# Kernel optimization log

Hardware: AMD Instinct MI355X
Metric: run time of the kernel (lower is better)

Reference implementation:

```python
import jax, jax.numpy as jnp
import numpy as np

N = 4096
IN_F = 512
OUT_F = 64
N_HEADS = 8
ALPHA = 0.2
NEG_INF = -9e15


def setup_inputs() -> dict:
    key = jax.random.key(0)
    k1, k2, k3, k4 = jax.random.split(key, 4)
    h = jax.random.normal(k1, (N, IN_F), dtype=jnp.float32)
    adj = jax.random.randint(k2, (N, N), 0, 2, dtype=jnp.int32)
    W = jax.random.normal(k3, (IN_F, OUT_F * N_HEADS), dtype=jnp.float32) * (1.414 / np.sqrt(IN_F))
    a = jax.random.normal(k4, (2 * OUT_F, 1), dtype=jnp.float32) * 0.1
    return {"h": h, "adj": adj, "W": W, "a": a}


def reference(h, adj, W, a):
    # Wh: [N, H, F]
    Wh = (h @ W).reshape(N, N_HEADS, OUT_F)
    # The all-pairs concat + matmul with a ([2F,1], shared across heads)
    # decomposes exactly: e[i,j,h] = leakyrelu(Wh[i,h]@a[:F] + Wh[j,h]@a[F:])
    a_src = a[:OUT_F, 0]
    a_dst = a[OUT_F:, 0]
    src = jnp.einsum('nhf,f->nh', Wh, a_src)  # [N, H]
    dst = jnp.einsum('nhf,f->nh', Wh, a_dst)  # [N, H]
    e = src[:, None, :] + dst[None, :, :]      # [N, N, H]
    e = jnp.where(e > 0, e, ALPHA * e)         # leaky relu
    e = jnp.where(adj[:, :, None] > 0, e, NEG_INF)
    attention = jax.nn.softmax(e, axis=1)      # softmax over neighbors j
    h_prime = jnp.einsum('ijh,jhf->ihf', attention, Wh)  # [N, H, F]
    out = h_prime.reshape(N, N_HEADS * OUT_F)
    return jax.nn.elu(out)
```

## Files before the change

kernel.cpp:

```cpp
#include <hip/hip_runtime.h>
#include <hip/hip_bf16.h>


typedef unsigned short ushort_t;
typedef __attribute__((ext_vector_type(8))) short bf16x8;
typedef __attribute__((ext_vector_type(4))) float f32x4;

#define LOG2E 1.4426950408889634f

__device__ __forceinline__ ushort_t f2bf(float x) {
    unsigned u = __builtin_bit_cast(unsigned, x);
    u += 0x7FFFu + ((u >> 16) & 1u);
    return (ushort_t)(u >> 16);
}

__global__ __launch_bounds__(256) void pack_adj(const int* __restrict__ adj,
                                                unsigned char* __restrict__ pk) {
    int wv = threadIdx.x >> 6, lane = threadIdx.x & 63;
    int row = blockIdx.x * 4 + wv;
    const int* ap = adj + (unsigned)row * 4096 + lane;
    unsigned char* pp = pk + (unsigned)row * 512;
    int jo = lane & 7;
#pragma unroll 2
    for (int k4 = 0; k4 < 16; k4++) {
        int v0 = ap[(k4 * 4 + 0) * 64];
        int v1 = ap[(k4 * 4 + 1) * 64];
        int v2 = ap[(k4 * 4 + 2) * 64];
        int v3 = ap[(k4 * 4 + 3) * 64];
        unsigned long long m0 = __ballot(v0 > 0);
        unsigned long long m1 = __ballot(v1 > 0);
        unsigned long long m2 = __ballot(v2 > 0);
        unsigned long long m3 = __ballot(v3 > 0);
        if (lane < 8) {
            int sh = jo * 8;
            unsigned b = ((unsigned)(m0 >> sh) & 0xFFu)
                       | (((unsigned)(m1 >> sh) & 0xFFu) << 8)
                       | (((unsigned)(m2 >> sh) & 0xFFu) << 16)
                       | (((unsigned)(m3 >> sh) & 0xFFu) << 24);
            *(unsigned*)(pp + jo * 64 + k4 * 4) = b;
        }
    }
}

__global__ __launch_bounds__(256) void transpose_w(const float* __restrict__ W,
                                                   ushort_t* __restrict__ WT) {
    __shared__ ushort_t t[32][33];
    int bx = blockIdx.x & 15, by = blockIdx.x >> 4;
    int tx = threadIdx.x & 31, ty = threadIdx.x >> 5;
#pragma unroll
    for (int i = 0; i < 32; i += 8)
        t[ty + i][tx] = f2bf(W[(by * 32 + ty + i) * 512 + bx * 32 + tx]);
    __syncthreads();
#pragma unroll
    for (int i = 0; i < 32; i += 8)
        WT[(bx * 32 + ty + i) * 512 + by * 32 + tx] = t[tx][ty + i];
}

__global__ __launch_bounds__(256, 4) void gemm_whT(const ushort_t* __restrict__ WT,
                                                   const float* __restrict__ h,
                                                   const float* __restrict__ a,
                                                   ushort_t* __restrict__ WhT,
                                                   float* __restrict__ expA,
                                                   float* __restrict__ expC,
                                                   float* __restrict__ expB,
                                                   float* __restrict__ expD) {
    __shared__ __align__(16) ushort_t Al[2][64][72];
    __shared__ __align__(16) ushort_t Bl[2][64][72];
    __shared__ float asrc[64], adst[64];
    __shared__ float sred[2][4][64];
    int tid = threadIdx.x;
    int wave = tid >> 6, lane = tid & 63, quad = lane >> 4, nn = lane & 15;
    int mb = blockIdx.x & 7, nb = blockIdx.x >> 3;
    if (tid < 64) {
        asrc[tid] = a[tid] * LOG2E;
        adst[tid] = a[64 + tid] * LOG2E;
    }
    int r = tid >> 2, s0 = tid & 3;
    const ushort_t* Ag = WT + (unsigned)((mb * 64 + r) * 512 + s0 * 8);
    const float* Bg = h + (unsigned)((nb * 64 + r) * 512 + s0 * 8);
    bf16x8 pA0 = *(const bf16x8*)(Ag);
    bf16x8 pA1 = *(const bf16x8*)(Ag + 32);
    float4 pb0 = *(const float4*)(Bg);
    float4 pb1 = *(const float4*)(Bg + 4);
    float4 pb2 = *(const float4*)(Bg + 32);
    float4 pb3 = *(const float4*)(Bg + 36);
    f32x4 acc[4] = {};
#pragma unroll 2
    for (int t = 0; t < 8; t++) {
        int cb = t & 1;
        *(bf16x8*)&Al[cb][r][s0 * 8] = pA0;
        *(bf16x8*)&Al[cb][r][s0 * 8 + 32] = pA1;
        bf16x8 bv;
        bv[0] = (short)f2bf(pb0.x); bv[1] = (short)f2bf(pb0.y);
        bv[2] = (short)f2bf(pb0.z); bv[3] = (short)f2bf(pb0.w);
        bv[4] = (short)f2bf(pb1.x); bv[5] = (short)f2bf(pb1.y);
        bv[6] = (short)f2bf(pb1.z); bv[7] = (short)f2bf(pb1.w);
        *(bf16x8*)&Bl[cb][r][s0 * 8] = bv;
        bv[0] = (short)f2bf(pb2.x); bv[1] = (short)f2bf(pb2.y);
        bv[2] = (short)f2bf(pb2.z); bv[3] = (short)f2bf(pb2.w);
        bv[4] = (short)f2bf(pb3.x); bv[5] = (short)f2bf(pb3.y);
        bv[6] = (short)f2bf(pb3.z); bv[7] = (short)f2bf(pb3.w);
        *(bf16x8*)&Bl[cb][r][s0 * 8 + 32] = bv;
        if (t < 7) {
            int ko = (t + 1) * 64;
            pA0 = *(const bf16x8*)(Ag + ko);
            pA1 = *(const bf16x8*)(Ag + ko + 32);
            pb0 = *(const float4*)(Bg + ko);
            pb1 = *(const float4*)(Bg + ko + 4);
            pb2 = *(const float4*)(Bg + ko + 32);
            pb3 = *(const float4*)(Bg + ko + 36);
        }
        if (t > 0) {
            int pb = cb ^ 1;
            bf16x8 af0 = *(const bf16x8*)&Al[pb][wave * 16 + nn][quad * 8];
            bf16x8 af1 = *(const bf16x8*)&Al[pb][wave * 16 + nn][32 + quad * 8];
#pragma unroll
            for (int nt = 0; nt < 4; nt++) {
                bf16x8 b0 = *(const bf16x8*)&Bl[pb][nt * 16 + nn][quad * 8];
                bf16x8 b1 = *(const bf16x8*)&Bl[pb][nt * 16 + nn][32 + quad * 8];
                acc[nt] = __builtin_amdgcn_mfma_f32_16x16x32_bf16(af0, b0, acc[nt], 0, 0, 0);
                acc[nt] = __builtin_amdgcn_mfma_f32_16x16x32_bf16(af1, b1, acc[nt], 0, 0, 0);
            }
        }
        __syncthreads();
    }
    {
        bf16x8 af0 = *(const bf16x8*)&Al[1][wave * 16 + nn][quad * 8];
        bf16x8 af1 = *(const bf16x8*)&Al[1][wave * 16 + nn][32 + quad * 8];
#pragma unroll
        for (int nt = 0; nt < 4; nt++) {
            bf16x8 b0 = *(const bf16x8*)&Bl[1][nt * 16 + nn][quad * 8];
            bf16x8 b1 = *(const bf16x8*)&Bl[1][nt * 16 + nn][32 + quad * 8];
            acc[nt] = __builtin_amdgcn_mfma_f32_16x16x32_bf16(af0, b0, acc[nt], 0, 0, 0);
            acc[nt] = __builtin_amdgcn_mfma_f32_16x16x32_bf16(af1, b1, acc[nt], 0, 0, 0);
        }
    }
    int row0 = mb * 64 + wave * 16 + quad * 4;
    int col0 = nb * 64 + nn;
    int f0i = wave * 16 + quad * 4;
#pragma unroll
    for (int nt = 0; nt < 4; nt++) {
        float s = 0.f, d = 0.f;
#pragma unroll
        for (int rr = 0; rr < 4; rr++) {
            float v = acc[nt][rr];
            WhT[(unsigned)((row0 + rr) * 4096 + col0 + nt * 16)] = f2bf(v);
            s += v * asrc[f0i + rr];
            d += v * adst[f0i + rr];
        }
        s += __shfl_xor(s, 16); s += __shfl_xor(s, 32);
        d += __shfl_xor(d, 16); d += __shfl_xor(d, 32);
        if (quad == 0) { sred[0][wave][nt * 16 + nn] = s; sred[1][wave][nt * 16 + nn] = d; }
    }
    __syncthreads();
    if (tid < 64) {
        float s = sred[0][0][tid] + sred[0][1][tid] + sred[0][2][tid] + sred[0][3][tid];
        unsigned idx = mb * 4096 + nb * 64 + tid;
        expA[idx] = __builtin_amdgcn_exp2f(s);
        expC[idx] = __builtin_amdgcn_exp2f(0.2f * s);
    } else if (tid < 128) {
        int c = tid - 64;
        float d = sred[1][0][c] + sred[1][1][c] + sred[1][2][c] + sred[1][3][c];
        unsigned idx = mb * 4096 + nb * 64 + c;
        expB[idx] = __builtin_amdgcn_exp2f(d);
        expD[idx] = __builtin_amdgcn_exp2f(0.2f * d);
    }
}

__global__ __launch_bounds__(512, 4) void gat_attn(const unsigned char* __restrict__ pk,
                                                   const ushort_t* __restrict__ WhT,
                                                   const float* __restrict__ expA,
                                                   const float* __restrict__ expC,
                                                   const float* __restrict__ expB,
                                                   const float* __restrict__ expD,
                                                   float* __restrict__ out) {
    __shared__ __align__(16) ushort_t Vb[2][128][72];
    __shared__ float denomp[2][2][32];
    int tid = threadIdx.x;
    int wave = tid >> 6, lane = tid & 63, quad = lane >> 4, nn = lane & 15;
    int hb = blockIdx.x >> 7, ib = blockIdx.x & 127;
    int i0 = ib * 32;
    int jhalf = wave >> 2, ws = wave & 3;
    int whead = ws >> 1, strip = ws & 1;
    int pi = strip * 16 + nn, jo = jhalf * 4 + quad;
    int head = hb * 2 + whead;
    float Ai = expA[head * 4096 + i0 + pi];
    float Ci = expC[head * 4096 + i0 + pi];
    const unsigned char* mp = pk + (unsigned)(i0 + pi) * 512 + jo * 64;
    const float* Bp = expB + (unsigned)head * 4096 + jo * 8;
    const float* Dp = expD + (unsigned)head * 4096 + jo * 8;
    int vr = tid >> 3, vcs = tid & 7;
    const ushort_t* Vg0 = WhT + (unsigned)(hb * 128 + vr) * 4096 + vcs * 8;
    const ushort_t* Vg1 = Vg0 + 64u * 4096u;
    bf16x8 onef;
#pragma unroll
    for (int i = 0; i < 8; i++) onef[i] = (short)0x3F80;
    f32x4 acc[4] = {};
    f32x4 accd = {};
    bf16x8 pv0 = *(const bf16x8*)(Vg0);
    bf16x8 pv1 = *(const bf16x8*)(Vg1);
    float4 pBD[2][4];
    pBD[0][0] = *(const float4*)(Bp);
    pBD[0][1] = *(const float4*)(Bp + 4);
    pBD[0][2] = *(const float4*)(Dp);
    pBD[0][3] = *(const float4*)(Dp + 4);
    unsigned mcur = *(const unsigned*)(mp);
    unsigned mnext = 0;
    for (int t = 0; t < 16; t++) {
#pragma unroll
        for (int u = 0; u < 4; u++) {
            int k = t * 4 + u;
            int cb = k & 1, pbuf = cb ^ 1;
            *(bf16x8*)&Vb[cb][vr][vcs * 8] = pv0;
            *(bf16x8*)&Vb[cb][64 + vr][vcs * 8] = pv1;
            float4 Bv0 = pBD[cb][0], Bv1 = pBD[cb][1];
            float4 Dv0 = pBD[cb][2], Dv1 = pBD[cb][3];
            unsigned w0, w1, w2, w3, w4, w5, w6, w7;
            {
                float w;
                w = fmaxf(Ai * Bv0.x, Ci * Dv0.x);
                w0 = __builtin_bit_cast(unsigned, w) & 0xFFFF0000u;
                w0 &= (unsigned)__builtin_amdgcn_sbfe(mcur, u * 8 + 0, 1);
                w = fmaxf(Ai * Bv0.y, Ci * Dv0.y);
                w1 = __builtin_bit_cast(unsigned, w) & 0xFFFF0000u;
                w1 &= (unsigned)__builtin_amdgcn_sbfe(mcur, u * 8 + 1, 1);
                w = fmaxf(Ai * Bv0.z, Ci * Dv0.z);
                w2 = __builtin_bit_cast(unsigned, w) & 0xFFFF0000u;
                w2 &= (unsigned)__builtin_amdgcn_sbfe(mcur, u * 8 + 2, 1);
                w = fmaxf(Ai * Bv0.w, Ci * Dv0.w);
                w3 = __builtin_bit_cast(unsigned, w) & 0xFFFF0000u;
                w3 &= (unsigned)__builtin_amdgcn_sbfe(mcur, u * 8 + 3, 1);
                w = fmaxf(Ai * Bv1.x, Ci * Dv1.x);
                w4 = __builtin_bit_cast(unsigned, w) & 0xFFFF0000u;
                w4 &= (unsigned)__builtin_amdgcn_sbfe(mcur, u * 8 + 4, 1);
                w = fmaxf(Ai * Bv1.y, Ci * Dv1.y);
                w5 = __builtin_bit_cast(unsigned, w) & 0xFFFF0000u;
                w5 &= (unsigned)__builtin_amdgcn_sbfe(mcur, u * 8 + 5, 1);
                w = fmaxf(Ai * Bv1.z, Ci * Dv1.z);
                w6 = __builtin_bit_cast(unsigned, w) & 0xFFFF0000u;
                w6 &= (unsigned)__builtin_amdgcn_sbfe(mcur, u * 8 + 6, 1);
                w = fmaxf(Ai * Bv1.w, Ci * Dv1.w);
                w7 = __builtin_bit_cast(unsigned, w) & 0xFFFF0000u;
                w7 &= (unsigned)__builtin_amdgcn_sbfe(mcur, u * 8 + 7, 1);
            }
            uint4 pq;
            pq.x = __builtin_amdgcn_perm(w1, w0, 0x07060302u);
            pq.y = __builtin_amdgcn_perm(w3, w2, 0x07060302u);
            pq.z = __builtin_amdgcn_perm(w5, w4, 0x07060302u);
            pq.w = __builtin_amdgcn_perm(w7, w6, 0x07060302u);
            bf16x8 af = __builtin_bit_cast(bf16x8, pq);
            if (u == 3) mcur = mnext;
            __syncthreads();
            __builtin_amdgcn_sched_barrier(0);
            if (k < 63) {
                pv0 = *(const bf16x8*)(Vg0 + (k + 1) * 64);
                pv1 = *(const bf16x8*)(Vg1 + (k + 1) * 64);
                pBD[pbuf][0] = *(const float4*)(Bp + (k + 1) * 64);
                pBD[pbuf][1] = *(const float4*)(Bp + (k + 1) * 64 + 4);
                pBD[pbuf][2] = *(const float4*)(Dp + (k + 1) * 64);
                pBD[pbuf][3] = *(const float4*)(Dp + (k + 1) * 64 + 4);
            }
            if (u == 0 && t < 15) mnext = *(const unsigned*)(mp + (t + 1) * 4);
#pragma unroll
            for (int nt = 0; nt < 4; nt++) {
                bf16x8 bv = *(const bf16x8*)&Vb[cb][whead * 64 + nt * 16 + nn][jhalf * 32 + quad * 8];
                acc[nt] = __builtin_amdgcn_mfma_f32_16x16x32_bf16(af, bv, acc[nt], 0, 0, 0);
            }
            accd = __builtin_amdgcn_mfma_f32_16x16x32_bf16(af, onef, accd, 0, 0, 0);
        }
    }
    if (nn == 0) {
#pragma unroll
        for (int rr = 0; rr < 4; rr++)
            denomp[jhalf][whead][strip * 16 + quad * 4 + rr] = accd[rr];
    }
    __syncthreads();
    float (*cmb)[64][8] = reinterpret_cast<float (*)[64][8]>(&Vb[0][0][0]);
    if (jhalf == 1) {
        *(f32x4*)&cmb[ws][lane][0] = acc[0];
        *(f32x4*)&cmb[ws][lane][4] = acc[1];
    }
    __syncthreads();
    if (jhalf == 0) {
        f32x4 o0 = acc[0] + *(const f32x4*)&cmb[ws][lane][0];
        f32x4 o1 = acc[1] + *(const f32x4*)&cmb[ws][lane][4];
#pragma unroll
        for (int rr = 0; rr < 4; rr++) {
            int il = strip * 16 + quad * 4 + rr;
            float dnm = fmaxf(denomp[0][whead][il] + denomp[1][whead][il], 1e-30f);
            float v0 = o0[rr] / dnm;
            float v1 = o1[rr] / dnm;
            v0 = v0 > 0.f ? v0 : __expf(v0) - 1.f;
            v1 = v1 > 0.f ? v1 : __expf(v1) - 1.f;
            unsigned oi = (unsigned)(i0 + il) * 512 + hb * 128 + whead * 64 + nn;
            out[oi] = v0;
            out[oi + 16] = v1;
        }
    }
    __syncthreads();
    if (jhalf == 1) {
        *(f32x4*)&cmb[ws][lane][0] = acc[2];
        *(f32x4*)&cmb[ws][lane][4] = acc[3];
    }
    __syncthreads();
    if (jhalf == 0) {
        f32x4 o0 = acc[2] + *(const f32x4*)&cmb[ws][lane][0];
        f32x4 o1 = acc[3] + *(const f32x4*)&cmb[ws][lane][4];
#pragma unroll
        for (int rr = 0; rr < 4; rr++) {
            int il = strip * 16 + quad * 4 + rr;
            float dnm = fmaxf(denomp[0][whead][il] + denomp[1][whead][il], 1e-30f);
            float v0 = o0[rr] / dnm;
            float v1 = o1[rr] / dnm;
            v0 = v0 > 0.f ? v0 : __expf(v0) - 1.f;
            v1 = v1 > 0.f ? v1 : __expf(v1) - 1.f;
            unsigned oi = (unsigned)(i0 + il) * 512 + hb * 128 + whead * 64 + 32 + nn;
            out[oi] = v0;
            out[oi + 16] = v1;
        }
    }
}

extern "C" void kernel_launch(void* const* d_in, const int* in_sizes, int n_in,
                              void* d_out, int out_size, void* d_ws, size_t ws_size,
                              hipStream_t stream) {
    const float* h   = (const float*)d_in[0];
    const int*   adj = (const int*)d_in[1];
    const float* W   = (const float*)d_in[2];
    const float* a   = (const float*)d_in[3];

    char* ws = (char*)d_ws;
    ushort_t* WhT = (ushort_t*)ws;
    ushort_t* WT  = (ushort_t*)(ws + (4u << 20));
    float* expA = (float*)(ws + (4u << 20) + (512u << 10));
    float* expC = expA + 8 * 4096;
    float* expB = expC + 8 * 4096;
    float* expD = expB + 8 * 4096;
    unsigned char* pkm = (unsigned char*)(ws + (5u << 20));

    pack_adj<<<1024, 256, 0, stream>>>(adj, pkm);
    transpose_w<<<256, 256, 0, stream>>>(W, WT);
    gemm_whT<<<512, 256, 0, stream>>>(WT, h, a, WhT, expA, expC, expB, expD);
    gat_attn<<<512, 512, 0, stream>>>(pkm, WhT, expA, expC, expB, expD,
                                      (float*)d_out);
}
```

Before: 175.6 us.

## Fuse adjacency packing into GEMM launch and widen attention j-tiles

```diff
diff --git a/kernel.cpp b/kernel.cpp
--- a/kernel.cpp
+++ b/kernel.cpp
@@ -12,34 +12,6 @@
     unsigned u = __builtin_bit_cast(unsigned, x);
     u += 0x7FFFu + ((u >> 16) & 1u);
     return (ushort_t)(u >> 16);
-}
-
-__global__ __launch_bounds__(256) void pack_adj(const int* __restrict__ adj,
-                                                unsigned char* __restrict__ pk) {
-    int wv = threadIdx.x >> 6, lane = threadIdx.x & 63;
-    int row = blockIdx.x * 4 + wv;
-    const int* ap = adj + (unsigned)row * 4096 + lane;
-    unsigned char* pp = pk + (unsigned)row * 512;
-    int jo = lane & 7;
-#pragma unroll 2
-    for (int k4 = 0; k4 < 16; k4++) {
-        int v0 = ap[(k4 * 4 + 0) * 64];
-        int v1 = ap[(k4 * 4 + 1) * 64];
-        int v2 = ap[(k4 * 4 + 2) * 64];
-        int v3 = ap[(k4 * 4 + 3) * 64];
-        unsigned long long m0 = __ballot(v0 > 0);
-        unsigned long long m1 = __ballot(v1 > 0);
-        unsigned long long m2 = __ballot(v2 > 0);
-        unsigned long long m3 = __ballot(v3 > 0);
-        if (lane < 8) {
-            int sh = jo * 8;
-            unsigned b = ((unsigned)(m0 >> sh) & 0xFFu)
-                       | (((unsigned)(m1 >> sh) & 0xFFu) << 8)
-                       | (((unsigned)(m2 >> sh) & 0xFFu) << 16)
-                       | (((unsigned)(m3 >> sh) & 0xFFu) << 24);
-            *(unsigned*)(pp + jo * 64 + k4 * 4) = b;
-        }
-    }
 }
 
 __global__ __launch_bounds__(256) void transpose_w(const float* __restrict__ W,
@@ -56,19 +28,48 @@
         WT[(bx * 32 + ty + i) * 512 + by * 32 + tx] = t[tx][ty + i];
 }
 
-__global__ __launch_bounds__(256, 4) void gemm_whT(const ushort_t* __restrict__ WT,
-                                                   const float* __restrict__ h,
-                                                   const float* __restrict__ a,
-                                                   ushort_t* __restrict__ WhT,
-                                                   float* __restrict__ expA,
-                                                   float* __restrict__ expC,
-                                                   float* __restrict__ expB,
-                                                   float* __restrict__ expD) {
+__global__ __launch_bounds__(256, 4) void gemm_pack(const ushort_t* __restrict__ WT,
+                                                    const float* __restrict__ h,
+                                                    const float* __restrict__ a,
+                                                    ushort_t* __restrict__ WhT,
+                                                    float* __restrict__ expA,
+                                                    float* __restrict__ expC,
+                                                    float* __restrict__ expB,
+                                                    float* __restrict__ expD,
+                                                    const int* __restrict__ adj,
+                                                    unsigned char* __restrict__ pk) {
     __shared__ __align__(16) ushort_t Al[2][64][72];
     __shared__ __align__(16) ushort_t Bl[2][64][72];
     __shared__ float asrc[64], adst[64];
     __shared__ float sred[2][4][64];
     int tid = threadIdx.x;
+    if (blockIdx.x >= 512) {
+        int pbid = blockIdx.x - 512;
+        int wv = tid >> 6, lane = tid & 63;
+        int row = pbid * 4 + wv;
+        const int* ap = adj + (unsigned)row * 4096 + lane;
+        unsigned char* pp = pk + (unsigned)row * 512;
+        int g = lane;
+        int sv = ((g >> 2) & 1) * 4 + (g & 3);
+        int cpar = g >> 3;
+#pragma unroll 2
+        for (int t = 0; t < 8; t++) {
+            unsigned long long m[8];
+#pragma unroll
+            for (int c8 = 0; c8 < 8; c8++)
+                m[c8] = __ballot(ap[(t * 8 + c8) * 64] > 0);
+            if (lane < 16) {
+                unsigned w = 0;
+#pragma unroll
+                for (int kq = 0; kq < 4; kq++) {
+                    unsigned b = (unsigned)(m[2 * kq + cpar] >> (8 * sv)) & 0xFFu;
+                    w |= b << (8 * kq);
+                }
+                *(unsigned*)(pp + g * 32 + t * 4) = w;
+            }
+        }
+        return;
+    }
     int wave = tid >> 6, lane = tid & 63, quad = lane >> 4, nn = lane & 15;
     int mb = blockIdx.x & 7, nb = blockIdx.x >> 3;
     if (tid < 64) {
@@ -174,149 +175,181 @@
                                                    const float* __restrict__ expB,
                                                    const float* __restrict__ expD,
                                                    float* __restrict__ out) {
-    __shared__ __align__(16) ushort_t Vb[2][128][72];
-    __shared__ float denomp[2][2][32];
+    __shared__ __align__(16) ushort_t Vb[2][128][136];
+    __shared__ float denomp[4][2][32];
     int tid = threadIdx.x;
     int wave = tid >> 6, lane = tid & 63, quad = lane >> 4, nn = lane & 15;
     int hb = blockIdx.x >> 7, ib = blockIdx.x & 127;
     int i0 = ib * 32;
-    int jhalf = wave >> 2, ws = wave & 3;
-    int whead = ws >> 1, strip = ws & 1;
-    int pi = strip * 16 + nn, jo = jhalf * 4 + quad;
+    int whead = wave & 1, jq = wave >> 1;
+    int g = jq * 4 + quad;
     int head = hb * 2 + whead;
-    float Ai = expA[head * 4096 + i0 + pi];
-    float Ci = expC[head * 4096 + i0 + pi];
-    const unsigned char* mp = pk + (unsigned)(i0 + pi) * 512 + jo * 64;
-    const float* Bp = expB + (unsigned)head * 4096 + jo * 8;
-    const float* Dp = expD + (unsigned)head * 4096 + jo * 8;
-    int vr = tid >> 3, vcs = tid & 7;
-    const ushort_t* Vg0 = WhT + (unsigned)(hb * 128 + vr) * 4096 + vcs * 8;
-    const ushort_t* Vg1 = Vg0 + 64u * 4096u;
+    float Ai0 = expA[head * 4096 + i0 + nn];
+    float Ci0 = expC[head * 4096 + i0 + nn];
+    float Ai1 = expA[head * 4096 + i0 + 16 + nn];
+    float Ci1 = expC[head * 4096 + i0 + 16 + nn];
+    const unsigned char* mpA = pk + (unsigned)(i0 + nn) * 512 + g * 32;
+    const unsigned char* mpB = mpA + 16 * 512;
+    const float* Bp = expB + (unsigned)head * 4096 + jq * 32 + quad * 8;
+    const float* Dp = expD + (unsigned)head * 4096 + jq * 32 + quad * 8;
+    int vrow = tid >> 2, vs = tid & 3;
+    const ushort_t* Vg = WhT + (unsigned)(hb * 128 + vrow) * 4096 + vs * 8;
     bf16x8 onef;
 #pragma unroll
     for (int i = 0; i < 8; i++) onef[i] = (short)0x3F80;
-    f32x4 acc[4] = {};
-    f32x4 accd = {};
-    bf16x8 pv0 = *(const bf16x8*)(Vg0);
-    bf16x8 pv1 = *(const bf16x8*)(Vg1);
-    float4 pBD[2][4];
-    pBD[0][0] = *(const float4*)(Bp);
-    pBD[0][1] = *(const float4*)(Bp + 4);
-    pBD[0][2] = *(const float4*)(Dp);
-    pBD[0][3] = *(const float4*)(Dp + 4);
-    unsigned mcur = *(const unsigned*)(mp);
-    unsigned mnext = 0;
-    for (int t = 0; t < 16; t++) {
+    f32x4 acc[2][4] = {};
+    f32x4 accd[2] = {};
+    bf16x8 pv[4];
+    float4 pBD[4];
+    pv[0] = *(const bf16x8*)(Vg);
+    pv[1] = *(const bf16x8*)(Vg + 32);
+    pv[2] = *(const bf16x8*)(Vg + 64);
+    pv[3] = *(const bf16x8*)(Vg + 96);
+    pBD[0] = *(const float4*)(Bp);
+    pBD[1] = *(const float4*)(Bp + 4);
+    pBD[2] = *(const float4*)(Dp);
+    pBD[3] = *(const float4*)(Dp + 4);
+    unsigned mcA = *(const unsigned*)(mpA);
+    unsigned mcB = *(const unsigned*)(mpB);
+    unsigned mnA = 0, mnB = 0;
+    for (int t = 0; t < 8; t++) {
 #pragma unroll
         for (int u = 0; u < 4; u++) {
-            int k = t * 4 + u;
-            int cb = k & 1, pbuf = cb ^ 1;
-            *(bf16x8*)&Vb[cb][vr][vcs * 8] = pv0;
-            *(bf16x8*)&Vb[cb][64 + vr][vcs * 8] = pv1;
-            float4 Bv0 = pBD[cb][0], Bv1 = pBD[cb][1];
-            float4 Dv0 = pBD[cb][2], Dv1 = pBD[cb][3];
-            unsigned w0, w1, w2, w3, w4, w5, w6, w7;
+            int kb = t * 4 + u;
+            int cb = kb & 1;
+            *(bf16x8*)&Vb[cb][vrow][vs * 8] = pv[0];
+            *(bf16x8*)&Vb[cb][vrow][vs * 8 + 32] = pv[1];
+            *(bf16x8*)&Vb[cb][vrow][vs * 8 + 64] = pv[2];
+            *(bf16x8*)&Vb[cb][vrow][vs * 8 + 96] = pv[3];
+            float4 Bv0 = pBD[0], Bv1 = pBD[1], Dv0 = pBD[2], Dv1 = pBD[3];
+            bf16x8 af0, af1;
             {
+                unsigned w0, w1, w2, w3, w4, w5, w6, w7;
                 float w;
-                w = fmaxf(Ai * Bv0.x, Ci * Dv0.x);
+                w = fmaxf(Ai0 * Bv0.x, Ci0 * Dv0.x);
                 w0 = __builtin_bit_cast(unsigned, w) & 0xFFFF0000u;
-                w0 &= (unsigned)__builtin_amdgcn_sbfe(mcur, u * 8 + 0, 1);
-                w = fmaxf(Ai * Bv0.y, Ci * Dv0.y);
+                w0 &= (unsigned)__builtin_amdgcn_sbfe(mcA, u * 8 + 0, 1);
+                w = fmaxf(Ai0 * Bv0.y, Ci0 * Dv0.y);
                 w1 = __builtin_bit_cast(unsigned, w) & 0xFFFF0000u;
-                w1 &= (unsigned)__builtin_amdgcn_sbfe(mcur, u * 8 + 1, 1);
-                w = fmaxf(Ai * Bv0.z, Ci * Dv0.z);
+                w1 &= (unsigned)__builtin_amdgcn_sbfe(mcA, u * 8 + 1, 1);
+                w = fmaxf(Ai0 * Bv0.z, Ci0 * Dv0.z);
                 w2 = __builtin_bit_cast(unsigned, w) & 0xFFFF0000u;
-                w2 &= (unsigned)__builtin_amdgcn_sbfe(mcur, u * 8 + 2, 1);
-                w = fmaxf(Ai * Bv0.w, Ci * Dv0.w);
+                w2 &= (unsigned)__builtin_amdgcn_sbfe(mcA, u * 8 + 2, 1);
+                w = fmaxf(Ai0 * Bv0.w, Ci0 * Dv0.w);
                 w3 = __builtin_bit_cast(unsigned, w) & 0xFFFF0000u;
-                w3 &= (unsigned)__builtin_amdgcn_sbfe(mcur, u * 8 + 3, 1);
-                w = fmaxf(Ai * Bv1.x, Ci * Dv1.x);
+                w3 &= (unsigned)__builtin_amdgcn_sbfe(mcA, u * 8 + 3, 1);
+                w = fmaxf(Ai0 * Bv1.x, Ci0 * Dv1.x);
                 w4 = __builtin_bit_cast(unsigned, w) & 0xFFFF0000u;
-                w4 &= (unsigned)__builtin_amdgcn_sbfe(mcur, u * 8 + 4, 1);
-                w = fmaxf(Ai * Bv1.y, Ci * Dv1.y);
+                w4 &= (unsigned)__builtin_amdgcn_sbfe(mcA, u * 8 + 4, 1);
+                w = fmaxf(Ai0 * Bv1.y, Ci0 * Dv1.y);
                 w5 = __builtin_bit_cast(unsigned, w) & 0xFFFF0000u;
-                w5 &= (unsigned)__builtin_amdgcn_sbfe(mcur, u * 8 + 5, 1);
-                w = fmaxf(Ai * Bv1.z, Ci * Dv1.z);
+                w5 &= (unsigned)__builtin_amdgcn_sbfe(mcA, u * 8 + 5, 1);
+                w = fmaxf(Ai0 * Bv1.z, Ci0 * Dv1.z);
                 w6 = __builtin_bit_cast(unsigned, w) & 0xFFFF0000u;
-                w6 &= (unsigned)__builtin_amdgcn_sbfe(mcur, u * 8 + 6, 1);
-                w = fmaxf(Ai * Bv1.w, Ci * Dv1.w);
+                w6 &= (unsigned)__builtin_amdgcn_sbfe(mcA, u * 8 + 6, 1);
+                w = fmaxf(Ai0 * Bv1.w, Ci0 * Dv1.w);
                 w7 = __builtin_bit_cast(unsigned, w) & 0xFFFF0000u;
-                w7 &= (unsigned)__builtin_amdgcn_sbfe(mcur, u * 8 + 7, 1);
-            }
-            uint4 pq;
-            pq.x = __builtin_amdgcn_perm(w1, w0, 0x07060302u);
-            pq.y = __builtin_amdgcn_perm(w3, w2, 0x07060302u);
-            pq.z = __builtin_amdgcn_perm(w5, w4, 0x07060302u);
-            pq.w = __builtin_amdgcn_perm(w7, w6, 0x07060302u);
-            bf16x8 af = __builtin_bit_cast(bf16x8, pq);
-            if (u == 3) mcur = mnext;
+                w7 &= (unsigned)__builtin_amdgcn_sbfe(mcA, u * 8 + 7, 1);
+                uint4 pq;
+                pq.x = __builtin_amdgcn_perm(w1, w0, 0x07060302u);
+                pq.y = __builtin_amdgcn_perm(w3, w2, 0x07060302u);
+                pq.z = __builtin_amdgcn_perm(w5, w4, 0x07060302u);
+                pq.w = __builtin_amdgcn_perm(w7, w6, 0x07060302u);
+                af0 = __builtin_bit_cast(bf16x8, pq);
+                w = fmaxf(Ai1 * Bv0.x, Ci1 * Dv0.x);
+                w0 = __builtin_bit_cast(unsigned, w) & 0xFFFF0000u;
+                w0 &= (unsigned)__builtin_amdgcn_sbfe(mcB, u * 8 + 0, 1);
+                w = fmaxf(Ai1 * Bv0.y, Ci1 * Dv0.y);
+                w1 = __builtin_bit_cast(unsigned, w) & 0xFFFF0000u;
+                w1 &= (unsigned)__builtin_amdgcn_sbfe(mcB, u * 8 + 1, 1);
+                w = fmaxf(Ai1 * Bv0.z, Ci1 * Dv0.z);
+                w2 = __builtin_bit_cast(unsigned, w) & 0xFFFF0000u;
+                w2 &= (unsigned)__builtin_amdgcn_sbfe(mcB, u * 8 + 2, 1);
+                w = fmaxf(Ai1 * Bv0.w, Ci1 * Dv0.w);
+                w3 = __builtin_bit_cast(unsigned, w) & 0xFFFF0000u;
+                w3 &= (unsigned)__builtin_amdgcn_sbfe(mcB, u * 8 + 3, 1);
+                w = fmaxf(Ai1 * Bv1.x, Ci1 * Dv1.x);
+                w4 = __builtin_bit_cast(unsigned, w) & 0xFFFF0000u;
+                w4 &= (unsigned)__builtin_amdgcn_sbfe(mcB, u * 8 + 4, 1);
+                w = fmaxf(Ai1 * Bv1.y, Ci1 * Dv1.y);
+                w5 = __builtin_bit_cast(unsigned, w) & 0xFFFF0000u;
+                w5 &= (unsigned)__builtin_amdgcn_sbfe(mcB, u * 8 + 5, 1);
+                w = fmaxf(Ai1 * Bv1.z, Ci1 * Dv1.z);
+                w6 = __builtin_bit_cast(unsigned, w) & 0xFFFF0000u;
+                w6 &= (unsigned)__builtin_amdgcn_sbfe(mcB, u * 8 + 6, 1);
+                w = fmaxf(Ai1 * Bv1.w, Ci1 * Dv1.w);
+                w7 = __builtin_bit_cast(unsigned, w) & 0xFFFF0000u;
+                w7 &= (unsigned)__builtin_amdgcn_sbfe(mcB, u * 8 + 7, 1);
+                pq.x = __builtin_amdgcn_perm(w1, w0, 0x07060302u);
+                pq.y = __builtin_amdgcn_perm(w3, w2, 0x07060302u);
+                pq.z = __builtin_amdgcn_perm(w5, w4, 0x07060302u);
+                pq.w = __builtin_amdgcn_perm(w7, w6, 0x07060302u);
+                af1 = __builtin_bit_cast(bf16x8, pq);
+            }
+            if (u == 3) { mcA = mnA; mcB = mnB; }
             __syncthreads();
             __builtin_amdgcn_sched_barrier(0);
-            if (k < 63) {
-                pv0 = *(const bf16x8*)(Vg0 + (k + 1) * 64);
-                pv1 = *(const bf16x8*)(Vg1 + (k + 1) * 64);
-                pBD[pbuf][0] = *(const float4*)(Bp + (k + 1) * 64);
-                pBD[pbuf][1] = *(const float4*)(Bp + (k + 1) * 64 + 4);
-                pBD[pbuf][2] = *(const float4*)(Dp + (k + 1) * 64);
-                pBD[pbuf][3] = *(const float4*)(Dp + (k + 1) * 64 + 4);
-            }
-            if (u == 0 && t < 15) mnext = *(const unsigned*)(mp + (t + 1) * 4);
+            if (kb < 31) {
+                const ushort_t* vp = Vg + (kb + 1) * 128;
+                pv[0] = *(const bf16x8*)(vp);
+                pv[1] = *(const bf16x8*)(vp + 32);
+                pv[2] = *(const bf16x8*)(vp + 64);
+                pv[3] = *(const bf16x8*)(vp + 96);
+                pBD[0] = *(const float4*)(Bp + (kb + 1) * 128);
+                pBD[1] = *(const float4*)(Bp + (kb + 1) * 128 + 4);
+                pBD[2] = *(const float4*)(Dp + (kb + 1) * 128);
+                pBD[3] = *(const float4*)(Dp + (kb + 1) * 128 + 4);
+            }
+            if (u == 0 && t < 7) {
+                mnA = *(const unsigned*)(mpA + (t + 1) * 4);
+                mnB = *(const unsigned*)(mpB + (t + 1) * 4);
+            }
 #pragma unroll
             for (int nt = 0; nt < 4; nt++) {
-                bf16x8 bv = *(const bf16x8*)&Vb[cb][whead * 64 + nt * 16 + nn][jhalf * 32 + quad * 8];
-                acc[nt] = __builtin_amdgcn_mfma_f32_16x16x32_bf16(af, bv, acc[nt], 0, 0, 0);
-            }
-            accd = __builtin_amdgcn_mfma_f32_16x16x32_bf16(af, onef, accd, 0, 0, 0);
-        }
-    }
+                bf16x8 bv = *(const bf16x8*)&Vb[cb][whead * 64 + nt * 16 + nn][jq * 32 + quad * 8];
+                acc[0][nt] = __builtin_amdgcn_mfma_f32_16x16x32_bf16(af0, bv, acc[0][nt], 0, 0, 0);
+                acc[1][nt] = __builtin_amdgcn_mfma_f32_16x16x32_bf16(af1, bv, acc[1][nt], 0, 0, 0);
+            }
+            accd[0] = __builtin_amdgcn_mfma_f32_16x16x32_bf16(af0, onef, accd[0], 0, 0, 0);
+            accd[1] = __builtin_amdgcn_mfma_f32_16x16x32_bf16(af1, onef, accd[1], 0, 0, 0);
+        }
+    }
+    __syncthreads();
     if (nn == 0) {
 #pragma unroll
-        for (int rr = 0; rr < 4; rr++)
-            denomp[jhalf][whead][strip * 16 + quad * 4 + rr] = accd[rr];
+        for (int s = 0; s < 2; s++)
+#pragma unroll
+            for (int rr = 0; rr < 4; rr++)
+                denomp[jq][whead][s * 16 + quad * 4 + rr] = accd[s][rr];
+    }
+    float (*cmb)[3][64][32] = reinterpret_cast<float (*)[3][64][32]>(&Vb[0][0][0]);
+    if (jq > 0) {
+#pragma unroll
+        for (int s = 0; s < 2; s++)
+#pragma unroll
+            for (int nt = 0; nt < 4; nt++)
+                *(f32x4*)&cmb[whead][jq - 1][lane][s * 16 + nt * 4] = acc[s][nt];
     }
     __syncthreads();
-    float (*cmb)[64][8] = reinterpret_cast<float (*)[64][8]>(&Vb[0][0][0]);
-    if (jhalf == 1) {
-        *(f32x4*)&cmb[ws][lane][0] = acc[0];
-        *(f32x4*)&cmb[ws][lane][4] = acc[1];
-    }
-    __syncthreads();
-    if (jhalf == 0) {
-        f32x4 o0 = acc[0] + *(const f32x4*)&cmb[ws][lane][0];
-        f32x4 o1 = acc[1] + *(const f32x4*)&cmb[ws][lane][4];
-#pragma unroll
-        for (int rr = 0; rr < 4; rr++) {
-            int il = strip * 16 + quad * 4 + rr;
-            float dnm = fmaxf(denomp[0][whead][il] + denomp[1][whead][il], 1e-30f);
-            float v0 = o0[rr] / dnm;
-            float v1 = o1[rr] / dnm;
-            v0 = v0 > 0.f ? v0 : __expf(v0) - 1.f;
-            v1 = v1 > 0.f ? v1 : __expf(v1) - 1.f;
-            unsigned oi = (unsigned)(i0 + il) * 512 + hb * 128 + whead * 64 + nn;
-            out[oi] = v0;
-            out[oi + 16] = v1;
-        }
-    }
-    __syncthreads();
-    if (jhalf == 1) {
-        *(f32x4*)&cmb[ws][lane][0] = acc[2];
-        *(f32x4*)&cmb[ws][lane][4] = acc[3];
-    }
-    __syncthreads();
-    if (jhalf == 0) {
-        f32x4 o0 = acc[2] + *(const f32x4*)&cmb[ws][lane][0];
-        f32x4 o1 = acc[3] + *(const f32x4*)&cmb[ws][lane][4];
-#pragma unroll
-        for (int rr = 0; rr < 4; rr++) {
-            int il = strip * 16 + quad * 4 + rr;
-            float dnm = fmaxf(denomp[0][whead][il] + denomp[1][whead][il], 1e-30f);
-            float v0 = o0[rr] / dnm;
-            float v1 = o1[rr] / dnm;
-            v0 = v0 > 0.f ? v0 : __expf(v0) - 1.f;
-            v1 = v1 > 0.f ? v1 : __expf(v1) - 1.f;
-            unsigned oi = (unsigned)(i0 + il) * 512 + hb * 128 + whead * 64 + 32 + nn;
-            out[oi] = v0;
-            out[oi + 16] = v1;
+    if (jq == 0) {
+#pragma unroll
+        for (int s = 0; s < 2; s++) {
+#pragma unroll
+            for (int nt = 0; nt < 4; nt++) {
+                f32x4 o = acc[s][nt]
+                        + *(const f32x4*)&cmb[whead][0][lane][s * 16 + nt * 4]
+                        + *(const f32x4*)&cmb[whead][1][lane][s * 16 + nt * 4]
+                        + *(const f32x4*)&cmb[whead][2][lane][s * 16 + nt * 4];
+#pragma unroll
+                for (int rr = 0; rr < 4; rr++) {
+                    int il = s * 16 + quad * 4 + rr;
+                    float dnm = fmaxf(denomp[0][whead][il] + denomp[1][whead][il]
+                                    + denomp[2][whead][il] + denomp[3][whead][il], 1e-30f);
+                    float v = o[rr] / dnm;
+                    v = v > 0.f ? v : __expf(v) - 1.f;
+                    out[(unsigned)(i0 + il) * 512 + hb * 128 + whead * 64 + nt * 16 + nn] = v;
+                }
+            }
         }
     }
 }
@@ -338,9 +371,9 @@
     float* expD = expB + 8 * 4096;
     unsigned char* pkm = (unsigned char*)(ws + (5u << 20));
 
-    pack_adj<<<1024, 256, 0, stream>>>(adj, pkm);
     transpose_w<<<256, 256, 0, stream>>>(W, WT);
-    gemm_whT<<<512, 256, 0, stream>>>(WT, h, a, WhT, expA, expC, expB, expD);
+    gemm_pack<<<1536, 256, 0, stream>>>(WT, h, a, WhT, expA, expC, expB, expD,
+                                        adj, pkm);
     gat_attn<<<512, 512, 0, stream>>>(pkm, WhT, expA, expC, expB, expD,
                                       (float*)d_out);
 }
```

New measurement: 168.8 us. 3.9% less time.

## Fuse adjacency packing into GEMM launch and shrink attention row tile to 16

Applied to the files above, without the earlier changes.

```diff
diff --git a/kernel.cpp b/kernel.cpp
--- a/kernel.cpp
+++ b/kernel.cpp
@@ -12,34 +12,6 @@
     unsigned u = __builtin_bit_cast(unsigned, x);
     u += 0x7FFFu + ((u >> 16) & 1u);
     return (ushort_t)(u >> 16);
-}
-
-__global__ __launch_bounds__(256) void pack_adj(const int* __restrict__ adj,
-                                                unsigned char* __restrict__ pk) {
-    int wv = threadIdx.x >> 6, lane = threadIdx.x & 63;
-    int row = blockIdx.x * 4 + wv;
-    const int* ap = adj + (unsigned)row * 4096 + lane;
-    unsigned char* pp = pk + (unsigned)row * 512;
-    int jo = lane & 7;
-#pragma unroll 2
-    for (int k4 = 0; k4 < 16; k4++) {
-        int v0 = ap[(k4 * 4 + 0) * 64];
-        int v1 = ap[(k4 * 4 + 1) * 64];
-        int v2 = ap[(k4 * 4 + 2) * 64];
-        int v3 = ap[(k4 * 4 + 3) * 64];
-        unsigned long long m0 = __ballot(v0 > 0);
-        unsigned long long m1 = __ballot(v1 > 0);
-        unsigned long long m2 = __ballot(v2 > 0);
-        unsigned long long m3 = __ballot(v3 > 0);
-        if (lane < 8) {
-            int sh = jo * 8;
-            unsigned b = ((unsigned)(m0 >> sh) & 0xFFu)
-                       | (((unsigned)(m1 >> sh) & 0xFFu) << 8)
-                       | (((unsigned)(m2 >> sh) & 0xFFu) << 16)
-                       | (((unsigned)(m3 >> sh) & 0xFFu) << 24);
-            *(unsigned*)(pp + jo * 64 + k4 * 4) = b;
-        }
-    }
 }
 
 __global__ __launch_bounds__(256) void transpose_w(const float* __restrict__ W,
@@ -56,19 +28,49 @@
         WT[(bx * 32 + ty + i) * 512 + by * 32 + tx] = t[tx][ty + i];
 }
 
-__global__ __launch_bounds__(256, 4) void gemm_whT(const ushort_t* __restrict__ WT,
-                                                   const float* __restrict__ h,
-                                                   const float* __restrict__ a,
-                                                   ushort_t* __restrict__ WhT,
-                                                   float* __restrict__ expA,
-                                                   float* __restrict__ expC,
-                                                   float* __restrict__ expB,
-                                                   float* __restrict__ expD) {
+__global__ __launch_bounds__(256, 4) void gemm_pack(const ushort_t* __restrict__ WT,
+                                                    const float* __restrict__ h,
+                                                    const float* __restrict__ a,
+                                                    ushort_t* __restrict__ WhT,
+                                                    float* __restrict__ expA,
+                                                    float* __restrict__ expC,
+                                                    float* __restrict__ expB,
+                                                    float* __restrict__ expD,
+                                                    const int* __restrict__ adj,
+                                                    unsigned char* __restrict__ pk) {
     __shared__ __align__(16) ushort_t Al[2][64][72];
     __shared__ __align__(16) ushort_t Bl[2][64][72];
     __shared__ float asrc[64], adst[64];
     __shared__ float sred[2][4][64];
     int tid = threadIdx.x;
+    if (blockIdx.x >= 512) {
+        int pbid = blockIdx.x - 512;
+        int wv = tid >> 6, lane = tid & 63;
+        int row = pbid * 4 + wv;
+        const int* ap = adj + (unsigned)row * 4096 + lane;
+        unsigned char* pp = pk + (unsigned)row * 512;
+        int jo = lane & 7;
+#pragma unroll 2
+        for (int k4 = 0; k4 < 16; k4++) {
+            int v0 = ap[(k4 * 4 + 0) * 64];
+            int v1 = ap[(k4 * 4 + 1) * 64];
+            int v2 = ap[(k4 * 4 + 2) * 64];
+            int v3 = ap[(k4 * 4 + 3) * 64];
+            unsigned long long m0 = __ballot(v0 > 0);
+            unsigned long long m1 = __ballot(v1 > 0);
+            unsigned long long m2 = __ballot(v2 > 0);
+            unsigned long long m3 = __ballot(v3 > 0);
+            if (lane < 8) {
+                int sh = jo * 8;
+                unsigned b = ((unsigned)(m0 >> sh) & 0xFFu)
+                           | (((unsigned)(m1 >> sh) & 0xFFu) << 8)
+                           | (((unsigned)(m2 >> sh) & 0xFFu) << 16)
+                           | (((unsigned)(m3 >> sh) & 0xFFu) << 24);
+                *(unsigned*)(pp + jo * 64 + k4 * 4) = b;
+            }
+        }
+        return;
+    }
     int wave = tid >> 6, lane = tid & 63, quad = lane >> 4, nn = lane & 15;
     int mb = blockIdx.x & 7, nb = blockIdx.x >> 3;
     if (tid < 64) {
@@ -167,7 +169,7 @@
     }
 }
 
-__global__ __launch_bounds__(512, 4) void gat_attn(const unsigned char* __restrict__ pk,
+__global__ __launch_bounds__(256, 4) void gat_attn(const unsigned char* __restrict__ pk,
                                                    const ushort_t* __restrict__ WhT,
                                                    const float* __restrict__ expA,
                                                    const float* __restrict__ expC,
@@ -175,30 +177,30 @@
                                                    const float* __restrict__ expD,
                                                    float* __restrict__ out) {
     __shared__ __align__(16) ushort_t Vb[2][128][72];
-    __shared__ float denomp[2][2][32];
+    __shared__ float denomp[2][2][16];
     int tid = threadIdx.x;
     int wave = tid >> 6, lane = tid & 63, quad = lane >> 4, nn = lane & 15;
-    int hb = blockIdx.x >> 7, ib = blockIdx.x & 127;
-    int i0 = ib * 32;
-    int jhalf = wave >> 2, ws = wave & 3;
-    int whead = ws >> 1, strip = ws & 1;
-    int pi = strip * 16 + nn, jo = jhalf * 4 + quad;
+    int hb = blockIdx.x >> 8, ib = blockIdx.x & 255;
+    int i0 = ib * 16;
+    int whead = wave & 1, jhalf = wave >> 1;
+    int jo = jhalf * 4 + quad;
     int head = hb * 2 + whead;
-    float Ai = expA[head * 4096 + i0 + pi];
-    float Ci = expC[head * 4096 + i0 + pi];
-    const unsigned char* mp = pk + (unsigned)(i0 + pi) * 512 + jo * 64;
+    float Ai = expA[head * 4096 + i0 + nn];
+    float Ci = expC[head * 4096 + i0 + nn];
+    const unsigned char* mp = pk + (unsigned)(i0 + nn) * 512 + jo * 64;
     const float* Bp = expB + (unsigned)head * 4096 + jo * 8;
     const float* Dp = expD + (unsigned)head * 4096 + jo * 8;
     int vr = tid >> 3, vcs = tid & 7;
-    const ushort_t* Vg0 = WhT + (unsigned)(hb * 128 + vr) * 4096 + vcs * 8;
-    const ushort_t* Vg1 = Vg0 + 64u * 4096u;
+    const ushort_t* Vg = WhT + (unsigned)(hb * 128 + vr) * 4096 + vcs * 8;
     bf16x8 onef;
 #pragma unroll
     for (int i = 0; i < 8; i++) onef[i] = (short)0x3F80;
     f32x4 acc[4] = {};
     f32x4 accd = {};
-    bf16x8 pv0 = *(const bf16x8*)(Vg0);
-    bf16x8 pv1 = *(const bf16x8*)(Vg1);
+    bf16x8 pv[4];
+#pragma unroll
+    for (int rr = 0; rr < 4; rr++)
+        pv[rr] = *(const bf16x8*)(Vg + rr * 32 * 4096);
     float4 pBD[2][4];
     pBD[0][0] = *(const float4*)(Bp);
     pBD[0][1] = *(const float4*)(Bp + 4);
@@ -211,8 +213,9 @@
         for (int u = 0; u < 4; u++) {
             int k = t * 4 + u;
             int cb = k & 1, pbuf = cb ^ 1;
-            *(bf16x8*)&Vb[cb][vr][vcs * 8] = pv0;
-            *(bf16x8*)&Vb[cb][64 + vr][vcs * 8] = pv1;
+#pragma unroll
+            for (int rr = 0; rr < 4; rr++)
+                *(bf16x8*)&Vb[cb][vr + rr * 32][vcs * 8] = pv[rr];
             float4 Bv0 = pBD[cb][0], Bv1 = pBD[cb][1];
             float4 Dv0 = pBD[cb][2], Dv1 = pBD[cb][3];
             unsigned w0, w1, w2, w3, w4, w5, w6, w7;
@@ -253,8 +256,10 @@
             __syncthreads();
             __builtin_amdgcn_sched_barrier(0);
             if (k < 63) {
-                pv0 = *(const bf16x8*)(Vg0 + (k + 1) * 64);
-                pv1 = *(const bf16x8*)(Vg1 + (k + 1) * 64);
+                const ushort_t* vp = Vg + (k + 1) * 64;
+#pragma unroll
+                for (int rr = 0; rr < 4; rr++)
+                    pv[rr] = *(const bf16x8*)(vp + rr * 32 * 4096);
                 pBD[pbuf][0] = *(const float4*)(Bp + (k + 1) * 64);
                 pBD[pbuf][1] = *(const float4*)(Bp + (k + 1) * 64 + 4);
                 pBD[pbuf][2] = *(const float4*)(Dp + (k + 1) * 64);
@@ -272,51 +277,28 @@
     if (nn == 0) {
 #pragma unroll
         for (int rr = 0; rr < 4; rr++)
-            denomp[jhalf][whead][strip * 16 + quad * 4 + rr] = accd[rr];
+            denomp[jhalf][whead][quad * 4 + rr] = accd[rr];
     }
     __syncthreads();
-    float (*cmb)[64][8] = reinterpret_cast<float (*)[64][8]>(&Vb[0][0][0]);
+    float (*cmb)[64][16] = reinterpret_cast<float (*)[64][16]>(&Vb[0][0][0]);
     if (jhalf == 1) {
-        *(f32x4*)&cmb[ws][lane][0] = acc[0];
-        *(f32x4*)&cmb[ws][lane][4] = acc[1];
+#pragma unroll
+        for (int nt = 0; nt < 4; nt++)
+            *(f32x4*)&cmb[whead][lane][nt * 4] = acc[nt];
     }
     __syncthreads();
     if (jhalf == 0) {
-        f32x4 o0 = acc[0] + *(const f32x4*)&cmb[ws][lane][0];
-        f32x4 o1 = acc[1] + *(const f32x4*)&cmb[ws][lane][4];
-#pragma unroll
-        for (int rr = 0; rr < 4; rr++) {
-            int il = strip * 16 + quad * 4 + rr;
-            float dnm = fmaxf(denomp[0][whead][il] + denomp[1][whead][il], 1e-30f);
-            float v0 = o0[rr] / dnm;
-            float v1 = o1[rr] / dnm;
-            v0 = v0 > 0.f ? v0 : __expf(v0) - 1.f;
-            v1 = v1 > 0.f ? v1 : __expf(v1) - 1.f;
-            unsigned oi = (unsigned)(i0 + il) * 512 + hb * 128 + whead * 64 + nn;
-            out[oi] = v0;
-            out[oi + 16] = v1;
-        }
-    }
-    __syncthreads();
-    if (jhalf == 1) {
-        *(f32x4*)&cmb[ws][lane][0] = acc[2];
-        *(f32x4*)&cmb[ws][lane][4] = acc[3];
-    }
-    __syncthreads();
-    if (jhalf == 0) {
-        f32x4 o0 = acc[2] + *(const f32x4*)&cmb[ws][lane][0];
-        f32x4 o1 = acc[3] + *(const f32x4*)&cmb[ws][lane][4];
-#pragma unroll
-        for (int rr = 0; rr < 4; rr++) {
-            int il = strip * 16 + quad * 4 + rr;
-            float dnm = fmaxf(denomp[0][whead][il] + denomp[1][whead][il], 1e-30f);
-            float v0 = o0[rr] / dnm;
-            float v1 = o1[rr] / dnm;
-            v0 = v0 > 0.f ? v0 : __expf(v0) - 1.f;
-            v1 = v1 > 0.f ? v1 : __expf(v1) - 1.f;
-            unsigned oi = (unsigned)(i0 + il) * 512 + hb * 128 + whead * 64 + 32 + nn;
-            out[oi] = v0;
-            out[oi + 16] = v1;
+#pragma unroll
+        for (int nt = 0; nt < 4; nt++) {
+            f32x4 o = acc[nt] + *(const f32x4*)&cmb[whead][lane][nt * 4];
+#pragma unroll
+            for (int rr = 0; rr < 4; rr++) {
+                int il = quad * 4 + rr;
+                float dnm = fmaxf(denomp[0][whead][il] + denomp[1][whead][il], 1e-30f);
+                float v = o[rr] / dnm;
+                v = v > 0.f ? v : __expf(v) - 1.f;
+                out[(unsigned)(i0 + il) * 512 + hb * 128 + whead * 64 + nt * 16 + nn] = v;
+            }
         }
     }
 }
@@ -338,9 +320,9 @@
     float* expD = expB + 8 * 4096;
     unsigned char* pkm = (unsigned char*)(ws + (5u << 20));
 
-    pack_adj<<<1024, 256, 0, stream>>>(adj, pkm);
     transpose_w<<<256, 256, 0, stream>>>(W, WT);
-    gemm_whT<<<512, 256, 0, stream>>>(WT, h, a, WhT, expA, expC, expB, expD);
-    gat_attn<<<512, 512, 0, stream>>>(pkm, WhT, expA, expC, expB, expD,
-                                      (float*)d_out);
-}
+    gemm_pack<<<1536, 256, 0, stream>>>(WT, h, a, WhT, expA, expC, expB, expD,
+                                        adj, pkm);
+    gat_attn<<<1024, 256, 0, stream>>>(pkm, WhT, expA, expC, expB, expD,
+                                       (float*)d_out);
+}
```

Result: slower. 194.7 us (+10.9%).

## Merge adjacency packing into GEMM launch and split attention blocks per head

Applied to the files above, without the earlier changes.

```diff
diff --git a/kernel.cpp b/kernel.cpp
--- a/kernel.cpp
+++ b/kernel.cpp
@@ -12,34 +12,6 @@
     unsigned u = __builtin_bit_cast(unsigned, x);
     u += 0x7FFFu + ((u >> 16) & 1u);
     return (ushort_t)(u >> 16);
-}
-
-__global__ __launch_bounds__(256) void pack_adj(const int* __restrict__ adj,
-                                                unsigned char* __restrict__ pk) {
-    int wv = threadIdx.x >> 6, lane = threadIdx.x & 63;
-    int row = blockIdx.x * 4 + wv;
-    const int* ap = adj + (unsigned)row * 4096 + lane;
-    unsigned char* pp = pk + (unsigned)row * 512;
-    int jo = lane & 7;
-#pragma unroll 2
-    for (int k4 = 0; k4 < 16; k4++) {
-        int v0 = ap[(k4 * 4 + 0) * 64];
-        int v1 = ap[(k4 * 4 + 1) * 64];
-        int v2 = ap[(k4 * 4 + 2) * 64];
-        int v3 = ap[(k4 * 4 + 3) * 64];
-        unsigned long long m0 = __ballot(v0 > 0);
-        unsigned long long m1 = __ballot(v1 > 0);
-        unsigned long long m2 = __ballot(v2 > 0);
-        unsigned long long m3 = __ballot(v3 > 0);
-        if (lane < 8) {
-            int sh = jo * 8;
-            unsigned b = ((unsigned)(m0 >> sh) & 0xFFu)
-                       | (((unsigned)(m1 >> sh) & 0xFFu) << 8)
-                       | (((unsigned)(m2 >> sh) & 0xFFu) << 16)
-                       | (((unsigned)(m3 >> sh) & 0xFFu) << 24);
-            *(unsigned*)(pp + jo * 64 + k4 * 4) = b;
-        }
-    }
 }
 
 __global__ __launch_bounds__(256) void transpose_w(const float* __restrict__ W,
@@ -56,19 +28,49 @@
         WT[(bx * 32 + ty + i) * 512 + by * 32 + tx] = t[tx][ty + i];
 }
 
-__global__ __launch_bounds__(256, 4) void gemm_whT(const ushort_t* __restrict__ WT,
-                                                   const float* __restrict__ h,
-                                                   const float* __restrict__ a,
-                                                   ushort_t* __restrict__ WhT,
-                                                   float* __restrict__ expA,
-                                                   float* __restrict__ expC,
-                                                   float* __restrict__ expB,
-                                                   float* __restrict__ expD) {
+__global__ __launch_bounds__(256, 4) void gemm_pack(const ushort_t* __restrict__ WT,
+                                                    const float* __restrict__ h,
+                                                    const float* __restrict__ a,
+                                                    ushort_t* __restrict__ WhT,
+                                                    float* __restrict__ expA,
+                                                    float* __restrict__ expC,
+                                                    float* __restrict__ expB,
+                                                    float* __restrict__ expD,
+                                                    const int* __restrict__ adj,
+                                                    unsigned char* __restrict__ pk) {
     __shared__ __align__(16) ushort_t Al[2][64][72];
     __shared__ __align__(16) ushort_t Bl[2][64][72];
     __shared__ float asrc[64], adst[64];
     __shared__ float sred[2][4][64];
     int tid = threadIdx.x;
+    if (blockIdx.x >= 512) {
+        int pbid = blockIdx.x - 512;
+        int wv = tid >> 6, lane = tid & 63;
+        int row = pbid * 4 + wv;
+        const int* ap = adj + (unsigned)row * 4096 + lane;
+        unsigned char* pp = pk + (unsigned)row * 512;
+        int jo = lane & 7;
+#pragma unroll 2
+        for (int k4 = 0; k4 < 16; k4++) {
+            int v0 = ap[(k4 * 4 + 0) * 64];
+            int v1 = ap[(k4 * 4 + 1) * 64];
+            int v2 = ap[(k4 * 4 + 2) * 64];
+            int v3 = ap[(k4 * 4 + 3) * 64];
+            unsigned long long m0 = __ballot(v0 > 0);
+            unsigned long long m1 = __ballot(v1 > 0);
+            unsigned long long m2 = __ballot(v2 > 0);
+            unsigned long long m3 = __ballot(v3 > 0);
+            if (lane < 8) {
+                int sh = jo * 8;
+                unsigned b = ((unsigned)(m0 >> sh) & 0xFFu)
+                           | (((unsigned)(m1 >> sh) & 0xFFu) << 8)
+                           | (((unsigned)(m2 >> sh) & 0xFFu) << 16)
+                           | (((unsigned)(m3 >> sh) & 0xFFu) << 24);
+                *(unsigned*)(pp + jo * 64 + k4 * 4) = b;
+            }
+        }
+        return;
+    }
     int wave = tid >> 6, lane = tid & 63, quad = lane >> 4, nn = lane & 15;
     int mb = blockIdx.x & 7, nb = blockIdx.x >> 3;
     if (tid < 64) {
@@ -167,31 +169,29 @@
     }
 }
 
-__global__ __launch_bounds__(512, 4) void gat_attn(const unsigned char* __restrict__ pk,
+__global__ __launch_bounds__(256, 6) void gat_attn(const unsigned char* __restrict__ pk,
                                                    const ushort_t* __restrict__ WhT,
                                                    const float* __restrict__ expA,
                                                    const float* __restrict__ expC,
                                                    const float* __restrict__ expB,
                                                    const float* __restrict__ expD,
                                                    float* __restrict__ out) {
-    __shared__ __align__(16) ushort_t Vb[2][128][72];
-    __shared__ float denomp[2][2][32];
+    __shared__ __align__(16) ushort_t Vb[2][64][72];
+    __shared__ float denomp[2][32];
     int tid = threadIdx.x;
     int wave = tid >> 6, lane = tid & 63, quad = lane >> 4, nn = lane & 15;
-    int hb = blockIdx.x >> 7, ib = blockIdx.x & 127;
+    int head = blockIdx.x >> 7, ib = blockIdx.x & 127;
     int i0 = ib * 32;
-    int jhalf = wave >> 2, ws = wave & 3;
-    int whead = ws >> 1, strip = ws & 1;
+    int strip = wave & 1, jhalf = wave >> 1;
     int pi = strip * 16 + nn, jo = jhalf * 4 + quad;
-    int head = hb * 2 + whead;
     float Ai = expA[head * 4096 + i0 + pi];
     float Ci = expC[head * 4096 + i0 + pi];
     const unsigned char* mp = pk + (unsigned)(i0 + pi) * 512 + jo * 64;
     const float* Bp = expB + (unsigned)head * 4096 + jo * 8;
     const float* Dp = expD + (unsigned)head * 4096 + jo * 8;
     int vr = tid >> 3, vcs = tid & 7;
-    const ushort_t* Vg0 = WhT + (unsigned)(hb * 128 + vr) * 4096 + vcs * 8;
-    const ushort_t* Vg1 = Vg0 + 64u * 4096u;
+    const ushort_t* Vg0 = WhT + (unsigned)(head * 64 + vr) * 4096 + vcs * 8;
+    const ushort_t* Vg1 = Vg0 + 32u * 4096u;
     bf16x8 onef;
 #pragma unroll
     for (int i = 0; i < 8; i++) onef[i] = (short)0x3F80;
@@ -212,7 +212,7 @@
             int k = t * 4 + u;
             int cb = k & 1, pbuf = cb ^ 1;
             *(bf16x8*)&Vb[cb][vr][vcs * 8] = pv0;
-            *(bf16x8*)&Vb[cb][64 + vr][vcs * 8] = pv1;
+            *(bf16x8*)&Vb[cb][32 + vr][vcs * 8] = pv1;
             float4 Bv0 = pBD[cb][0], Bv1 = pBD[cb][1];
             float4 Dv0 = pBD[cb][2], Dv1 = pBD[cb][3];
             unsigned w0, w1, w2, w3, w4, w5, w6, w7;
@@ -263,7 +263,7 @@
             if (u == 0 && t < 15) mnext = *(const unsigned*)(mp + (t + 1) * 4);
 #pragma unroll
             for (int nt = 0; nt < 4; nt++) {
-                bf16x8 bv = *(const bf16x8*)&Vb[cb][whead * 64 + nt * 16 + nn][jhalf * 32 + quad * 8];
+                bf16x8 bv = *(const bf16x8*)&Vb[cb][nt * 16 + nn][jhalf * 32 + quad * 8];
                 acc[nt] = __builtin_amdgcn_mfma_f32_16x16x32_bf16(af, bv, acc[nt], 0, 0, 0);
             }
             accd = __builtin_amdgcn_mfma_f32_16x16x32_bf16(af, onef, accd, 0, 0, 0);
@@ -272,49 +272,49 @@
     if (nn == 0) {
 #pragma unroll
         for (int rr = 0; rr < 4; rr++)
-            denomp[jhalf][whead][strip * 16 + quad * 4 + rr] = accd[rr];
+            denomp[jhalf][strip * 16 + quad * 4 + rr] = accd[rr];
     }
     __syncthreads();
     float (*cmb)[64][8] = reinterpret_cast<float (*)[64][8]>(&Vb[0][0][0]);
     if (jhalf == 1) {
-        *(f32x4*)&cmb[ws][lane][0] = acc[0];
-        *(f32x4*)&cmb[ws][lane][4] = acc[1];
+        *(f32x4*)&cmb[strip][lane][0] = acc[0];
+        *(f32x4*)&cmb[strip][lane][4] = acc[1];
     }
     __syncthreads();
     if (jhalf == 0) {
-        f32x4 o0 = acc[0] + *(const f32x4*)&cmb[ws][lane][0];
-        f32x4 o1 = acc[1] + *(const f32x4*)&cmb[ws][lane][4];
+        f32x4 o0 = acc[0] + *(const f32x4*)&cmb[strip][lane][0];
+        f32x4 o1 = acc[1] + *(const f32x4*)&cmb[strip][lane][4];
 #pragma unroll
         for (int rr = 0; rr < 4; rr++) {
             int il = strip * 16 + quad * 4 + rr;
-            float dnm = fmaxf(denomp[0][whead][il] + denomp[1][whead][il], 1e-30f);
+            float dnm = fmaxf(denomp[0][il] + denomp[1][il], 1e-30f);
             float v0 = o0[rr] / dnm;
             float v1 = o1[rr] / dnm;
             v0 = v0 > 0.f ? v0 : __expf(v0) - 1.f;
             v1 = v1 > 0.f ? v1 : __expf(v1) - 1.f;
-            unsigned oi = (unsigned)(i0 + il) * 512 + hb * 128 + whead * 64 + nn;
+            unsigned oi = (unsigned)(i0 + il) * 512 + head * 64 + nn;
             out[oi] = v0;
             out[oi + 16] = v1;
         }
     }
     __syncthreads();
     if (jhalf == 1) {
-        *(f32x4*)&cmb[ws][lane][0] = acc[2];
-        *(f32x4*)&cmb[ws][lane][4] = acc[3];
+        *(f32x4*)&cmb[strip][lane][0] = acc[2];
+        *(f32x4*)&cmb[strip][lane][4] = acc[3];
     }
     __syncthreads();
     if (jhalf == 0) {
-        f32x4 o0 = acc[2] + *(const f32x4*)&cmb[ws][lane][0];
-        f32x4 o1 = acc[3] + *(const f32x4*)&cmb[ws][lane][4];
+        f32x4 o0 = acc[2] + *(const f32x4*)&cmb[strip][lane][0];
+        f32x4 o1 = acc[3] + *(const f32x4*)&cmb[strip][lane][4];
 #pragma unroll
         for (int rr = 0; rr < 4; rr++) {
             int il = strip * 16 + quad * 4 + rr;
-            float dnm = fmaxf(denomp[0][whead][il] + denomp[1][whead][il], 1e-30f);
+            float dnm = fmaxf(denomp[0][il] + denomp[1][il], 1e-30f);
             float v0 = o0[rr] / dnm;
             float v1 = o1[rr] / dnm;
             v0 = v0 > 0.f ? v0 : __expf(v0) - 1.f;
             v1 = v1 > 0.f ? v1 : __expf(v1) - 1.f;
-            unsigned oi = (unsigned)(i0 + il) * 512 + hb * 128 + whead * 64 + 32 + nn;
+            unsigned oi = (unsigned)(i0 + il) * 512 + head * 64 + 32 + nn;
             out[oi] = v0;
             out[oi + 16] = v1;
         }
@@ -338,9 +338,9 @@
     float* expD = expB + 8 * 4096;
     unsigned char* pkm = (unsigned char*)(ws + (5u << 20));
 
-    pack_adj<<<1024, 256, 0, stream>>>(adj, pkm);
     transpose_w<<<256, 256, 0, stream>>>(W, WT);
-    gemm_whT<<<512, 256, 0, stream>>>(WT, h, a, WhT, expA, expC, expB, expD);
-    gat_attn<<<512, 512, 0, stream>>>(pkm, WhT, expA, expC, expB, expD,
-                                      (float*)d_out);
-}
+    gemm_pack<<<1536, 256, 0, stream>>>(WT, h, a, WhT, expA, expC, expB, expD,
+                                        adj, pkm);
+    gat_attn<<<1024, 256, 0, stream>>>(pkm, WhT, expA, expC, expB, expD,
+                                       (float*)d_out);
+}
```

New measurement: 183.0 us. 1.04x slower.
